# Kernel tuning notes

Measured on AMD Instinct MI355X. Metric: run time of the kernel, lower is better.

The kernel has to match this reference:

```python
import jax, jax.numpy as jnp
import numpy as np

N, D, F1, F2, F3, H = 4096, 512, 64, 32, 16, 4
ALPHA = 0.2  # LeakyReLU negative slope
NEG = -9e15


def setup_inputs() -> dict:
    key = jax.random.key(0)
    ks = jax.random.split(key, 11)
    # sparse binary adjacency with self loops (adj.to_dense() in original)
    adj = (jax.random.uniform(ks[1], (N, N)) < 0.01).astype(jnp.float32)
    adj = jnp.maximum(adj, jnp.eye(N, dtype=jnp.float32))
    return {
        "x": jax.random.normal(ks[0], (N, D), jnp.float32),
        "adj": adj,
        "W_heads": jax.random.normal(ks[2], (H, D, F1), jnp.float32) * 0.05,
        "a_heads": jax.random.normal(ks[3], (H, 2 * F1, 1), jnp.float32) * 0.05,
        "W_att": jax.random.normal(ks[4], (H * F1, F1), jnp.float32) * 0.05,
        "a_att": jax.random.normal(ks[5], (2 * F1, 1), jnp.float32) * 0.05,
        "W1": jax.random.normal(ks[6], (F1, F2), jnp.float32) * 0.05,
        "W2": jax.random.normal(ks[7], (F2, F3), jnp.float32) * 0.05,
        "W3": jax.random.normal(ks[8], (F2, F3), jnp.float32) * 0.05,
        "eps": jax.random.normal(ks[9], (N, F3), jnp.float32),
    }


def _gat(x, adj, W, a, out_dim):
    Wh = x @ W                                   # [N, F]
    e = (Wh @ a[:out_dim]) + (Wh @ a[out_dim:]).T  # [N,1] + [1,N] -> [N,N]
    e = jax.nn.leaky_relu(e, negative_slope=ALPHA)
    att = jax.nn.softmax(jnp.where(adj > 0, e, NEG), axis=-1)
    return jax.nn.elu(att @ Wh)                  # [N, F]


def reference(x, adj, W_heads, a_heads, W_att, a_att, W1, W2, W3, eps):
    # multi-head GAT, concat along feature dim
    heads = jax.vmap(lambda W, a: _gat(x, adj, W, a, F1))(W_heads, a_heads)  # [H,N,F1]
    cat = jnp.transpose(heads, (1, 0, 2)).reshape(N, H * F1)
    gc_att = _gat(cat, adj, W_att, a_att, F1)    # [N, F1]
    # GCN layers (dropout off, no bias): spmm(adj, x @ W)
    h1 = jax.nn.relu(adj @ (gc_att @ W1))        # [N, F2]
    mu = adj @ (h1 @ W2)                         # [N, F3]
    logvar = adj @ (h1 @ W3)                     # [N, F3]
    # reparameterize (vae_bool=True): eps * exp(logvar) + mu
    z = eps * jnp.exp(logvar) + mu
    adj_rec = z @ z.T                            # inner-product decoder [N,N]
    return adj_rec, mu, logvar
```

## Files before the change

### kernel.cpp

```cpp
#include <hip/hip_runtime.h>
#include <math.h>

#define NN 4096
#define DD 512
#define F1 64
#define F2 32
#define F3 16
#define NH 4
#define ALPHA 0.2f
#define CAP 160

__global__ void k_csr(const float* __restrict__ adj, int* __restrict__ colidx,
                      int* __restrict__ deg) {
  __shared__ int cnt;
  int i = blockIdx.x, tid = threadIdx.x;
  if (tid == 0) cnt = 0;
  __syncthreads();
  const float4* arow = (const float4*)(adj + (size_t)i * NN);
  for (int t = tid; t < NN / 4; t += 256) {
    float4 v = arow[t];
    int base = t * 4;
    if (v.x != 0.f) { int p = atomicAdd(&cnt, 1); if (p < CAP) colidx[(size_t)i * CAP + p] = base; }
    if (v.y != 0.f) { int p = atomicAdd(&cnt, 1); if (p < CAP) colidx[(size_t)i * CAP + p] = base + 1; }
    if (v.z != 0.f) { int p = atomicAdd(&cnt, 1); if (p < CAP) colidx[(size_t)i * CAP + p] = base + 2; }
    if (v.w != 0.f) { int p = atomicAdd(&cnt, 1); if (p < CAP) colidx[(size_t)i * CAP + p] = base + 3; }
  }
  __syncthreads();
  if (tid == 0) deg[i] = cnt < CAP ? cnt : CAP;
}

__global__ void k_wh_heads(const float* __restrict__ x,
                           const float* __restrict__ W_heads,
                           const float* __restrict__ a_heads,
                           float* __restrict__ Whcat,
                           float* __restrict__ s1,
                           float* __restrict__ s2) {
  const int ROWS = 4;
  __shared__ float xs[ROWS][DD];
  int tid = threadIdx.x;
  int r0 = blockIdx.x * ROWS;
  const float4* xsrc = (const float4*)(x + (size_t)r0 * DD);
  for (int t = tid; t < ROWS * DD / 4; t += 256) ((float4*)xs)[t] = xsrc[t];
  __syncthreads();
  int h = tid >> 6;
  int f = tid & 63;
  const float* W = W_heads + (size_t)h * DD * F1 + f;
  float acc[ROWS] = {0.f, 0.f, 0.f, 0.f};
  for (int k = 0; k < DD; k += 4) {
    float w0 = W[(k + 0) * F1];
    float w1 = W[(k + 1) * F1];
    float w2 = W[(k + 2) * F1];
    float w3 = W[(k + 3) * F1];
#pragma unroll
    for (int r = 0; r < ROWS; ++r) {
      float4 xv = *(const float4*)&xs[r][k];
      acc[r] = fmaf(xv.x, w0, acc[r]);
      acc[r] = fmaf(xv.y, w1, acc[r]);
      acc[r] = fmaf(xv.z, w2, acc[r]);
      acc[r] = fmaf(xv.w, w3, acc[r]);
    }
  }
  float a1 = a_heads[h * 2 * F1 + f];
  float a2 = a_heads[h * 2 * F1 + F1 + f];
#pragma unroll
  for (int r = 0; r < ROWS; ++r) {
    Whcat[(size_t)(r0 + r) * (NH * F1) + tid] = acc[r];
    float v1 = acc[r] * a1;
    float v2 = acc[r] * a2;
#pragma unroll
    for (int off = 32; off > 0; off >>= 1) {
      v1 += __shfl_down(v1, off, 64);
      v2 += __shfl_down(v2, off, 64);
    }
    if (f == 0) {
      s1[h * NN + r0 + r] = v1;
      s2[h * NN + r0 + r] = v2;
    }
  }
}

__global__ void k_gat_heads(const int* __restrict__ colidx, const int* __restrict__ deg,
                            const float* __restrict__ Whcat,
                            const float* __restrict__ s1, const float* __restrict__ s2,
                            float* __restrict__ cat) {
  __shared__ int idx[CAP];
  __shared__ float s2s[NH][CAP];
  int i = blockIdx.x, tid = threadIdx.x;
  int c = deg[i];
  for (int t = tid; t < c; t += 256) idx[t] = colidx[(size_t)i * CAP + t];
  __syncthreads();
  int h = tid >> 6;
  int f = tid & 63;
  const float* s2h = s2 + h * NN;
  for (int k = f; k < c; k += 64) s2s[h][k] = s2h[idx[k]];
  __syncthreads();
  float s1v = s1[h * NN + i];
  float M = -INFINITY;
  for (int k = f; k < c; k += 64) M = fmaxf(M, s2s[h][k]);
#pragma unroll
  for (int off = 32; off > 0; off >>= 1) M = fmaxf(M, __shfl_down(M, off, 64));
  M = __shfl(M, 0, 64);
  float e0 = s1v + M;
  float m = (e0 >= 0.f) ? e0 : ALPHA * e0;
  float acc = 0.f, l = 0.f;
  for (int k = 0; k < c; ++k) {
    int j = idx[k];
    float e = s1v + s2s[h][k];
    e = (e >= 0.f) ? e : ALPHA * e;
    float w = __expf(e - m);
    l += w;
    acc = fmaf(w, Whcat[(size_t)j * (NH * F1) + tid], acc);
  }
  float o = acc / l;
  cat[(size_t)i * (NH * F1) + tid] = (o > 0.f) ? o : expm1f(o);
}

__global__ void k_wh2(const float* __restrict__ cat,
                      const float* __restrict__ W_att,
                      const float* __restrict__ a_att,
                      float* __restrict__ Wh2,
                      float* __restrict__ s1b, float* __restrict__ s2b) {
  const int ROWS = 8;
  __shared__ float cs[ROWS][NH * F1];
  int tid = threadIdx.x;
  int r0 = blockIdx.x * ROWS;
  const float4* csrc = (const float4*)(cat + (size_t)r0 * 256);
  for (int t = tid; t < ROWS * 256 / 4; t += 256) ((float4*)cs)[t] = csrc[t];
  __syncthreads();
  int g = tid >> 6;
  int f = tid & 63;
  float a1 = a_att[f], a2 = a_att[64 + f];
  const float* W = W_att + f;
#pragma unroll
  for (int rr = 0; rr < 2; ++rr) {
    int r = g * 2 + rr;
    float acc = 0.f;
    for (int k = 0; k < 256; k += 4) {
      float4 cv = *(const float4*)&cs[r][k];
      acc = fmaf(cv.x, W[(k + 0) * 64], acc);
      acc = fmaf(cv.y, W[(k + 1) * 64], acc);
      acc = fmaf(cv.z, W[(k + 2) * 64], acc);
      acc = fmaf(cv.w, W[(k + 3) * 64], acc);
    }
    Wh2[(size_t)(r0 + r) * 64 + f] = acc;
    float v1 = acc * a1, v2 = acc * a2;
#pragma unroll
    for (int off = 32; off > 0; off >>= 1) {
      v1 += __shfl_down(v1, off, 64);
      v2 += __shfl_down(v2, off, 64);
    }
    if (f == 0) { s1b[r0 + r] = v1; s2b[r0 + r] = v2; }
  }
}

__global__ void k_gat2(const int* __restrict__ colidx, const int* __restrict__ deg,
                       const float* __restrict__ Wh2,
                       const float* __restrict__ s1b, const float* __restrict__ s2b,
                       float* __restrict__ gc) {
  __shared__ int idx[4][CAP];
  int w = threadIdx.x >> 6, f = threadIdx.x & 63;
  int i = blockIdx.x * 4 + w;
  int c = deg[i];
  for (int k = f; k < c; k += 64) idx[w][k] = colidx[(size_t)i * CAP + k];
  __syncthreads();
  float s1v = s1b[i];
  float M = -INFINITY;
  for (int k = f; k < c; k += 64) M = fmaxf(M, s2b[idx[w][k]]);
#pragma unroll
  for (int off = 32; off > 0; off >>= 1) M = fmaxf(M, __shfl_down(M, off, 64));
  M = __shfl(M, 0, 64);
  float e0 = s1v + M;
  float m = (e0 >= 0.f) ? e0 : ALPHA * e0;
  float acc = 0.f, l = 0.f;
  for (int k = 0; k < c; ++k) {
    int j = idx[w][k];
    float e = s1v + s2b[j];
    e = (e >= 0.f) ? e : ALPHA * e;
    float wt = __expf(e - m);
    l += wt;
    acc = fmaf(wt, Wh2[(size_t)j * 64 + f], acc);
  }
  float o = acc / l;
  gc[(size_t)i * 64 + f] = (o > 0.f) ? o : expm1f(o);
}

__global__ void k_t1(const float* __restrict__ gc, const float* __restrict__ W1,
                     float* __restrict__ t1) {
  const int ROWS = 8;
  __shared__ float gs[ROWS][64];
  int tid = threadIdx.x;
  int r0 = blockIdx.x * ROWS;
  const float4* gsrc = (const float4*)(gc + (size_t)r0 * 64);
  for (int t = tid; t < ROWS * 64 / 4; t += 256) ((float4*)gs)[t] = gsrc[t];
  __syncthreads();
  int r = tid >> 5, f = tid & 31;
  float acc = 0.f;
  for (int k = 0; k < 64; ++k) acc = fmaf(gs[r][k], W1[k * 32 + f], acc);
  t1[(size_t)(r0 + r) * 32 + f] = acc;
}

__global__ void k_gcn1(const int* __restrict__ colidx, const int* __restrict__ deg,
                       const float* __restrict__ t1, float* __restrict__ h1) {
  __shared__ int idx[8][CAP];
  int tid = threadIdx.x;
  int r = tid >> 5, lane = tid & 31;
  int i = blockIdx.x * 8 + r;
  int c = deg[i];
  for (int k = lane; k < c; k += 32) idx[r][k] = colidx[(size_t)i * CAP + k];
  __syncthreads();
  float acc = 0.f;
  for (int k = 0; k < c; ++k) acc += t1[(size_t)idx[r][k] * 32 + lane];
  h1[(size_t)i * 32 + lane] = fmaxf(acc, 0.f);
}

__global__ void k_t23(const float* __restrict__ h1, const float* __restrict__ W2,
                      const float* __restrict__ W3, float* __restrict__ t23) {
  const int ROWS = 8;
  __shared__ float hs[ROWS][32];
  int tid = threadIdx.x;
  int r0 = blockIdx.x * ROWS;
  const float4* hsrc = (const float4*)(h1 + (size_t)r0 * 32);
  for (int t = tid; t < ROWS * 32 / 4; t += 256) ((float4*)hs)[t] = hsrc[t];
  __syncthreads();
  int r = tid >> 5, f = tid & 31;
  const float* W = (f < 16) ? (W2 + f) : (W3 + (f - 16));
  float acc = 0.f;
  for (int k = 0; k < F2; ++k) acc = fmaf(hs[r][k], W[k * 16], acc);
  t23[(size_t)(r0 + r) * 32 + f] = acc;
}

__global__ void k_gcn2(const int* __restrict__ colidx, const int* __restrict__ deg,
                       const float* __restrict__ t23, const float* __restrict__ eps,
                       float* __restrict__ mu_out, float* __restrict__ lv_out,
                       float* __restrict__ z) {
  __shared__ int idx[8][CAP];
  int tid = threadIdx.x;
  int r = tid >> 5, g = tid & 31;
  int i = blockIdx.x * 8 + r;
  int c = deg[i];
  for (int k = g; k < c; k += 32) idx[r][k] = colidx[(size_t)i * CAP + k];
  __syncthreads();
  float acc = 0.f;
  for (int k = 0; k < c; ++k) acc += t23[(size_t)idx[r][k] * 32 + g];
  float lvv = __shfl(acc, (threadIdx.x & 63) + 16, 64);
  if (g < 16) {
    mu_out[(size_t)i * 16 + g] = acc;
    z[(size_t)i * 16 + g] = eps[(size_t)i * 16 + g] * expf(lvv) + acc;
  } else {
    lv_out[(size_t)i * 16 + (g - 16)] = acc;
  }
}

__global__ void k_zzt(const float* __restrict__ z, float* __restrict__ out) {
  __shared__ float zr[64][17];
  __shared__ float zc[64][17];
  int bj = blockIdx.x, bi = blockIdx.y;
  int tid = threadIdx.x;
  for (int t = tid; t < 64 * 16; t += 256) {
    zr[t >> 4][t & 15] = z[(size_t)(bi * 64 + (t >> 4)) * 16 + (t & 15)];
    zc[t >> 4][t & 15] = z[(size_t)(bj * 64 + (t >> 4)) * 16 + (t & 15)];
  }
  __syncthreads();
  int cthr = tid & 63;
  int rbase = (tid >> 6) * 16;
  for (int r = rbase; r < rbase + 16; ++r) {
    float acc = 0.f;
#pragma unroll
    for (int k = 0; k < 16; ++k) acc = fmaf(zr[r][k], zc[cthr][k], acc);
    out[(size_t)(bi * 64 + r) * NN + bj * 64 + cthr] = acc;
  }
}

extern "C" void kernel_launch(void* const* d_in, const int* in_sizes, int n_in,
                              void* d_out, int out_size, void* d_ws, size_t ws_size,
                              hipStream_t stream) {
  const float* x       = (const float*)d_in[0];
  const float* adj     = (const float*)d_in[1];
  const float* W_heads = (const float*)d_in[2];
  const float* a_heads = (const float*)d_in[3];
  const float* W_att   = (const float*)d_in[4];
  const float* a_att   = (const float*)d_in[5];
  const float* W1      = (const float*)d_in[6];
  const float* W2      = (const float*)d_in[7];
  const float* W3      = (const float*)d_in[8];
  const float* eps     = (const float*)d_in[9];

  float* out = (float*)d_out;
  float* adj_rec = out;
  float* mu_out  = out + (size_t)NN * NN;
  float* lv_out  = mu_out + (size_t)NN * F3;

  float* ws = (float*)d_ws;
  float* Whcat = ws;               ws += (size_t)NN * NH * F1;
  float* s1    = ws;               ws += (size_t)NH * NN;
  float* s2    = ws;               ws += (size_t)NH * NN;
  float* cat   = ws;               ws += (size_t)NN * NH * F1;
  float* Wh2   = ws;               ws += (size_t)NN * F1;
  float* s1b   = ws;               ws += NN;
  float* s2b   = ws;               ws += NN;
  float* gc    = ws;               ws += (size_t)NN * F1;
  float* t1    = ws;               ws += (size_t)NN * F2;
  float* h1    = ws;               ws += (size_t)NN * F2;
  float* t23   = ws;               ws += (size_t)NN * 2 * F3;
  float* z     = ws;               ws += (size_t)NN * F3;
  int*   colidx = (int*)ws;        ws += (size_t)NN * CAP;
  int*   deg    = (int*)ws;        ws += NN;

  k_csr<<<NN, 256, 0, stream>>>(adj, colidx, deg);
  k_wh_heads<<<NN / 4, 256, 0, stream>>>(x, W_heads, a_heads, Whcat, s1, s2);
  k_gat_heads<<<NN, 256, 0, stream>>>(colidx, deg, Whcat, s1, s2, cat);
  k_wh2<<<NN / 8, 256, 0, stream>>>(cat, W_att, a_att, Wh2, s1b, s2b);
  k_gat2<<<NN / 4, 256, 0, stream>>>(colidx, deg, Wh2, s1b, s2b, gc);
  k_t1<<<NN / 8, 256, 0, stream>>>(gc, W1, t1);
  k_gcn1<<<NN / 8, 256, 0, stream>>>(colidx, deg, t1, h1);
  k_t23<<<NN / 8, 256, 0, stream>>>(h1, W2, W3, t23);
  k_gcn2<<<NN / 8, 256, 0, stream>>>(colidx, deg, t23, eps, mu_out, lv_out, z);
  k_zzt<<<dim3(64, 64), 256, 0, stream>>>(z, adj_rec);
}
```

Baseline: 255.5 us.

## Fuse GAT/GCN stages, transpose head weights, and register-tile the decoder

Adds a kernel that transposes W_heads so the head projection can read contiguous float4 weights. The projection now runs 512-thread blocks with a split-K reduction through shared memory. The GAT kernels precompute softmax weights cooperatively and use four independent accumulators in the gather. The second GAT is fused with the W1 projection, and the first GCN with the W2/W3 projection, which removes two launches and two intermediate buffers. The z·zᵀ decoder uses 4x4 register tiles with float4 stores to cut the cost of writing the large output. An extra transpose launch is added in exchange.

```diff
diff --git a/kernel.cpp b/kernel.cpp
--- a/kernel.cpp
+++ b/kernel.cpp
@@ -10,6 +10,24 @@
 #define ALPHA 0.2f
 #define CAP 160
 
+__device__ __forceinline__ float lrelu(float e) { return (e >= 0.f) ? e : ALPHA * e; }
+
+__global__ void k_wtr(const float* __restrict__ W, float* __restrict__ Wt) {
+  __shared__ float tile[64][65];
+  int h = blockIdx.x >> 3;
+  int kt = (blockIdx.x & 7) * 64;
+  int tid = threadIdx.x;
+  for (int t = tid; t < 4096; t += 256) {
+    int kk = t >> 6, ff = t & 63;
+    tile[kk][ff] = W[(size_t)h * DD * F1 + (size_t)(kt + kk) * F1 + ff];
+  }
+  __syncthreads();
+  for (int t = tid; t < 4096; t += 256) {
+    int ff = t >> 6, kk = t & 63;
+    Wt[(size_t)(h * F1 + ff) * DD + kt + kk] = tile[kk][ff];
+  }
+}
+
 __global__ void k_csr(const float* __restrict__ adj, int* __restrict__ colidx,
                       int* __restrict__ deg) {
   __shared__ int cnt;
@@ -29,52 +47,88 @@
   if (tid == 0) deg[i] = cnt < CAP ? cnt : CAP;
 }
 
-__global__ void k_wh_heads(const float* __restrict__ x,
-                           const float* __restrict__ W_heads,
-                           const float* __restrict__ a_heads,
-                           float* __restrict__ Whcat,
-                           float* __restrict__ s1,
-                           float* __restrict__ s2) {
-  const int ROWS = 4;
-  __shared__ float xs[ROWS][DD];
-  int tid = threadIdx.x;
-  int r0 = blockIdx.x * ROWS;
+__global__ __launch_bounds__(512) void k_wh_heads(
+    const float* __restrict__ x, const float* __restrict__ Wt,
+    const float* __restrict__ a_heads, float* __restrict__ Whcat,
+    float* __restrict__ s1, float* __restrict__ s2) {
+  __shared__ float xs[8 * DD];
+  int tid = threadIdx.x;
+  int r0 = blockIdx.x * 8;
   const float4* xsrc = (const float4*)(x + (size_t)r0 * DD);
-  for (int t = tid; t < ROWS * DD / 4; t += 256) ((float4*)xs)[t] = xsrc[t];
-  __syncthreads();
-  int h = tid >> 6;
+  float4* xd = (float4*)xs;
+  xd[tid] = xsrc[tid];
+  xd[tid + 512] = xsrc[tid + 512];
+  __syncthreads();
   int f = tid & 63;
-  const float* W = W_heads + (size_t)h * DD * F1 + f;
-  float acc[ROWS] = {0.f, 0.f, 0.f, 0.f};
-  for (int k = 0; k < DD; k += 4) {
-    float w0 = W[(k + 0) * F1];
-    float w1 = W[(k + 1) * F1];
-    float w2 = W[(k + 2) * F1];
-    float w3 = W[(k + 3) * F1];
-#pragma unroll
-    for (int r = 0; r < ROWS; ++r) {
-      float4 xv = *(const float4*)&xs[r][k];
-      acc[r] = fmaf(xv.x, w0, acc[r]);
-      acc[r] = fmaf(xv.y, w1, acc[r]);
-      acc[r] = fmaf(xv.z, w2, acc[r]);
-      acc[r] = fmaf(xv.w, w3, acc[r]);
+  int rg = (tid >> 6) & 3;
+  int ks = tid >> 8;
+  int k0 = ks * 256;
+  const float* wp0 = Wt + (size_t)(0 * F1 + f) * DD;
+  const float* wp1 = Wt + (size_t)(1 * F1 + f) * DD;
+  const float* wp2 = Wt + (size_t)(2 * F1 + f) * DD;
+  const float* wp3 = Wt + (size_t)(3 * F1 + f) * DD;
+  const float* xa = xs + (size_t)(rg * 2) * DD;
+  const float* xb = xa + DD;
+  float acc[2][4] = {{0.f,0.f,0.f,0.f},{0.f,0.f,0.f,0.f}};
+  for (int k = k0; k < k0 + 256; k += 4) {
+    float4 wv[4];
+    wv[0] = *(const float4*)(wp0 + k);
+    wv[1] = *(const float4*)(wp1 + k);
+    wv[2] = *(const float4*)(wp2 + k);
+    wv[3] = *(const float4*)(wp3 + k);
+    float4 va = *(const float4*)(xa + k);
+    float4 vb = *(const float4*)(xb + k);
+#pragma unroll
+    for (int h = 0; h < 4; ++h) {
+      acc[0][h] = fmaf(va.x, wv[h].x, acc[0][h]);
+      acc[0][h] = fmaf(va.y, wv[h].y, acc[0][h]);
+      acc[0][h] = fmaf(va.z, wv[h].z, acc[0][h]);
+      acc[0][h] = fmaf(va.w, wv[h].w, acc[0][h]);
+      acc[1][h] = fmaf(vb.x, wv[h].x, acc[1][h]);
+      acc[1][h] = fmaf(vb.y, wv[h].y, acc[1][h]);
+      acc[1][h] = fmaf(vb.z, wv[h].z, acc[1][h]);
+      acc[1][h] = fmaf(vb.w, wv[h].w, acc[1][h]);
     }
   }
-  float a1 = a_heads[h * 2 * F1 + f];
-  float a2 = a_heads[h * 2 * F1 + F1 + f];
-#pragma unroll
-  for (int r = 0; r < ROWS; ++r) {
-    Whcat[(size_t)(r0 + r) * (NH * F1) + tid] = acc[r];
-    float v1 = acc[r] * a1;
-    float v2 = acc[r] * a2;
-#pragma unroll
-    for (int off = 32; off > 0; off >>= 1) {
-      v1 += __shfl_down(v1, off, 64);
-      v2 += __shfl_down(v2, off, 64);
-    }
-    if (f == 0) {
-      s1[h * NN + r0 + r] = v1;
-      s2[h * NN + r0 + r] = v2;
+  __syncthreads();
+  float* pbuf = xs;
+  if (ks == 1) {
+    int t = tid & 255;
+#pragma unroll
+    for (int r = 0; r < 2; ++r)
+#pragma unroll
+      for (int h = 0; h < 4; ++h) pbuf[t * 8 + r * 4 + h] = acc[r][h];
+  }
+  __syncthreads();
+  if (ks == 0) {
+#pragma unroll
+    for (int r = 0; r < 2; ++r)
+#pragma unroll
+      for (int h = 0; h < 4; ++h) acc[r][h] += pbuf[tid * 8 + r * 4 + h];
+    int rb = r0 + rg * 2;
+#pragma unroll
+    for (int r = 0; r < 2; ++r)
+#pragma unroll
+      for (int h = 0; h < 4; ++h)
+        Whcat[(size_t)(rb + r) * (NH * F1) + h * 64 + f] = acc[r][h];
+#pragma unroll
+    for (int h = 0; h < 4; ++h) {
+      float a1 = a_heads[h * 2 * F1 + f];
+      float a2 = a_heads[h * 2 * F1 + F1 + f];
+#pragma unroll
+      for (int r = 0; r < 2; ++r) {
+        float v1 = acc[r][h] * a1;
+        float v2 = acc[r][h] * a2;
+#pragma unroll
+        for (int off = 32; off > 0; off >>= 1) {
+          v1 += __shfl_down(v1, off, 64);
+          v2 += __shfl_down(v2, off, 64);
+        }
+        if (f == 0) {
+          s1[h * NN + rb + r] = v1;
+          s2[h * NN + rb + r] = v2;
+        }
+      }
     }
   }
 }
@@ -84,7 +138,7 @@
                             const float* __restrict__ s1, const float* __restrict__ s2,
                             float* __restrict__ cat) {
   __shared__ int idx[CAP];
-  __shared__ float s2s[NH][CAP];
+  __shared__ float wsh[NH][CAP];
   int i = blockIdx.x, tid = threadIdx.x;
   int c = deg[i];
   for (int t = tid; t < c; t += 256) idx[t] = colidx[(size_t)i * CAP + t];
@@ -92,26 +146,39 @@
   int h = tid >> 6;
   int f = tid & 63;
   const float* s2h = s2 + h * NN;
-  for (int k = f; k < c; k += 64) s2s[h][k] = s2h[idx[k]];
-  __syncthreads();
   float s1v = s1[h * NN + i];
   float M = -INFINITY;
-  for (int k = f; k < c; k += 64) M = fmaxf(M, s2s[h][k]);
+  for (int k = f; k < c; k += 64) {
+    float v = s2h[idx[k]];
+    wsh[h][k] = v;
+    M = fmaxf(M, v);
+  }
 #pragma unroll
   for (int off = 32; off > 0; off >>= 1) M = fmaxf(M, __shfl_down(M, off, 64));
   M = __shfl(M, 0, 64);
-  float e0 = s1v + M;
-  float m = (e0 >= 0.f) ? e0 : ALPHA * e0;
-  float acc = 0.f, l = 0.f;
-  for (int k = 0; k < c; ++k) {
-    int j = idx[k];
-    float e = s1v + s2s[h][k];
-    e = (e >= 0.f) ? e : ALPHA * e;
-    float w = __expf(e - m);
-    l += w;
-    acc = fmaf(w, Whcat[(size_t)j * (NH * F1) + tid], acc);
-  }
-  float o = acc / l;
+  float m = lrelu(s1v + M);
+  float lsum = 0.f;
+  for (int k = f; k < c; k += 64) {
+    float w = __expf(lrelu(s1v + wsh[h][k]) - m);
+    wsh[h][k] = w;
+    lsum += w;
+  }
+#pragma unroll
+  for (int off = 32; off > 0; off >>= 1) lsum += __shfl_down(lsum, off, 64);
+  float linv = 1.f / __shfl(lsum, 0, 64);
+  __syncthreads();
+  const float* base = Whcat + h * 64 + f;
+  float a0 = 0.f, a1 = 0.f, a2 = 0.f, a3 = 0.f;
+  int k = 0;
+  for (; k + 4 <= c; k += 4) {
+    int j0 = idx[k], j1 = idx[k + 1], j2 = idx[k + 2], j3 = idx[k + 3];
+    a0 = fmaf(wsh[h][k],     base[(size_t)j0 * 256], a0);
+    a1 = fmaf(wsh[h][k + 1], base[(size_t)j1 * 256], a1);
+    a2 = fmaf(wsh[h][k + 2], base[(size_t)j2 * 256], a2);
+    a3 = fmaf(wsh[h][k + 3], base[(size_t)j3 * 256], a3);
+  }
+  for (; k < c; ++k) a0 = fmaf(wsh[h][k], base[(size_t)idx[k] * 256], a0);
+  float o = (a0 + a1 + a2 + a3) * linv;
   cat[(size_t)i * (NH * F1) + tid] = (o > 0.f) ? o : expm1f(o);
 }
 
@@ -153,101 +220,129 @@
   }
 }
 
-__global__ void k_gat2(const int* __restrict__ colidx, const int* __restrict__ deg,
-                       const float* __restrict__ Wh2,
-                       const float* __restrict__ s1b, const float* __restrict__ s2b,
-                       float* __restrict__ gc) {
-  __shared__ int idx[4][CAP];
-  int w = threadIdx.x >> 6, f = threadIdx.x & 63;
+__global__ void k_gat2t1(const int* __restrict__ colidx, const int* __restrict__ deg,
+                         const float* __restrict__ Wh2,
+                         const float* __restrict__ s1b, const float* __restrict__ s2b,
+                         const float* __restrict__ W1, float* __restrict__ t1) {
+  __shared__ int idx4[4][CAP];
+  __shared__ float wsh4[4][CAP];
+  __shared__ float grow[4][64];
+  __shared__ float W1s[F1 * F2];
+  int tid = threadIdx.x;
+  int w = tid >> 6, f = tid & 63;
   int i = blockIdx.x * 4 + w;
   int c = deg[i];
-  for (int k = f; k < c; k += 64) idx[w][k] = colidx[(size_t)i * CAP + k];
+  for (int t = tid; t < F1 * F2; t += 256) W1s[t] = W1[t];
+  for (int k = f; k < c; k += 64) idx4[w][k] = colidx[(size_t)i * CAP + k];
   __syncthreads();
   float s1v = s1b[i];
   float M = -INFINITY;
-  for (int k = f; k < c; k += 64) M = fmaxf(M, s2b[idx[w][k]]);
+  for (int k = f; k < c; k += 64) {
+    float v = s2b[idx4[w][k]];
+    wsh4[w][k] = v;
+    M = fmaxf(M, v);
+  }
 #pragma unroll
   for (int off = 32; off > 0; off >>= 1) M = fmaxf(M, __shfl_down(M, off, 64));
   M = __shfl(M, 0, 64);
-  float e0 = s1v + M;
-  float m = (e0 >= 0.f) ? e0 : ALPHA * e0;
-  float acc = 0.f, l = 0.f;
-  for (int k = 0; k < c; ++k) {
-    int j = idx[w][k];
-    float e = s1v + s2b[j];
-    e = (e >= 0.f) ? e : ALPHA * e;
-    float wt = __expf(e - m);
-    l += wt;
-    acc = fmaf(wt, Wh2[(size_t)j * 64 + f], acc);
-  }
-  float o = acc / l;
-  gc[(size_t)i * 64 + f] = (o > 0.f) ? o : expm1f(o);
-}
-
-__global__ void k_t1(const float* __restrict__ gc, const float* __restrict__ W1,
-                     float* __restrict__ t1) {
-  const int ROWS = 8;
-  __shared__ float gs[ROWS][64];
-  int tid = threadIdx.x;
-  int r0 = blockIdx.x * ROWS;
-  const float4* gsrc = (const float4*)(gc + (size_t)r0 * 64);
-  for (int t = tid; t < ROWS * 64 / 4; t += 256) ((float4*)gs)[t] = gsrc[t];
-  __syncthreads();
-  int r = tid >> 5, f = tid & 31;
-  float acc = 0.f;
-  for (int k = 0; k < 64; ++k) acc = fmaf(gs[r][k], W1[k * 32 + f], acc);
-  t1[(size_t)(r0 + r) * 32 + f] = acc;
-}
-
-__global__ void k_gcn1(const int* __restrict__ colidx, const int* __restrict__ deg,
-                       const float* __restrict__ t1, float* __restrict__ h1) {
-  __shared__ int idx[8][CAP];
-  int tid = threadIdx.x;
-  int r = tid >> 5, lane = tid & 31;
-  int i = blockIdx.x * 8 + r;
+  float m = lrelu(s1v + M);
+  float lsum = 0.f;
+  for (int k = f; k < c; k += 64) {
+    float wv = __expf(lrelu(s1v + wsh4[w][k]) - m);
+    wsh4[w][k] = wv;
+    lsum += wv;
+  }
+#pragma unroll
+  for (int off = 32; off > 0; off >>= 1) lsum += __shfl_down(lsum, off, 64);
+  float linv = 1.f / __shfl(lsum, 0, 64);
+  __syncthreads();
+  const float* base = Wh2 + f;
+  float a0 = 0.f, a1 = 0.f, a2 = 0.f, a3 = 0.f;
+  int k = 0;
+  for (; k + 4 <= c; k += 4) {
+    int j0 = idx4[w][k], j1 = idx4[w][k + 1], j2 = idx4[w][k + 2], j3 = idx4[w][k + 3];
+    a0 = fmaf(wsh4[w][k],     base[(size_t)j0 * 64], a0);
+    a1 = fmaf(wsh4[w][k + 1], base[(size_t)j1 * 64], a1);
+    a2 = fmaf(wsh4[w][k + 2], base[(size_t)j2 * 64], a2);
+    a3 = fmaf(wsh4[w][k + 3], base[(size_t)j3 * 64], a3);
+  }
+  for (; k < c; ++k) a0 = fmaf(wsh4[w][k], base[(size_t)idx4[w][k] * 64], a0);
+  float o = (a0 + a1 + a2 + a3) * linv;
+  grow[w][f] = (o > 0.f) ? o : expm1f(o);
+  __syncthreads();
+  if (f < F2) {
+    float acc = 0.f;
+#pragma unroll 8
+    for (int kk = 0; kk < F1; ++kk) acc = fmaf(grow[w][kk], W1s[kk * F2 + f], acc);
+    t1[(size_t)i * F2 + f] = acc;
+  }
+}
+
+__global__ void k_gcn1t23(const int* __restrict__ colidx, const int* __restrict__ deg,
+                          const float* __restrict__ t1,
+                          const float* __restrict__ W2, const float* __restrict__ W3,
+                          float* __restrict__ t23) {
+  __shared__ int idx4[4][CAP];
+  __shared__ float hrow[4][F2];
+  __shared__ float Wc[F2 * 32];
+  int tid = threadIdx.x;
+  int w = tid >> 6, lane = tid & 63;
+  int nb = lane >> 5, g = lane & 31;
+  int i = blockIdx.x * 4 + w;
   int c = deg[i];
-  for (int k = lane; k < c; k += 32) idx[r][k] = colidx[(size_t)i * CAP + k];
-  __syncthreads();
-  float acc = 0.f;
-  for (int k = 0; k < c; ++k) acc += t1[(size_t)idx[r][k] * 32 + lane];
-  h1[(size_t)i * 32 + lane] = fmaxf(acc, 0.f);
-}
-
-__global__ void k_t23(const float* __restrict__ h1, const float* __restrict__ W2,
-                      const float* __restrict__ W3, float* __restrict__ t23) {
-  const int ROWS = 8;
-  __shared__ float hs[ROWS][32];
-  int tid = threadIdx.x;
-  int r0 = blockIdx.x * ROWS;
-  const float4* hsrc = (const float4*)(h1 + (size_t)r0 * 32);
-  for (int t = tid; t < ROWS * 32 / 4; t += 256) ((float4*)hs)[t] = hsrc[t];
-  __syncthreads();
-  int r = tid >> 5, f = tid & 31;
-  const float* W = (f < 16) ? (W2 + f) : (W3 + (f - 16));
-  float acc = 0.f;
-  for (int k = 0; k < F2; ++k) acc = fmaf(hs[r][k], W[k * 16], acc);
-  t23[(size_t)(r0 + r) * 32 + f] = acc;
+  for (int t = tid; t < F2 * 32; t += 256) {
+    int kk = t >> 5, gg = t & 31;
+    Wc[t] = (gg < 16) ? W2[kk * 16 + gg] : W3[kk * 16 + (gg - 16)];
+  }
+  for (int k = lane; k < c; k += 64) idx4[w][k] = colidx[(size_t)i * CAP + k];
+  __syncthreads();
+  float a0 = 0.f, a1 = 0.f;
+  int k = nb;
+  for (; k + 2 < c; k += 4) {
+    a0 += t1[(size_t)idx4[w][k] * F2 + g];
+    a1 += t1[(size_t)idx4[w][k + 2] * F2 + g];
+  }
+  for (; k < c; k += 2) a0 += t1[(size_t)idx4[w][k] * F2 + g];
+  float tot = a0 + a1;
+  tot += __shfl_xor(tot, 32, 64);
+  float h1v = fmaxf(tot, 0.f);
+  if (nb == 0) hrow[w][g] = h1v;
+  __syncthreads();
+  if (lane < 32) {
+    float acc = 0.f;
+#pragma unroll 8
+    for (int kk = 0; kk < F2; ++kk) acc = fmaf(hrow[w][kk], Wc[kk * 32 + lane], acc);
+    t23[(size_t)i * 32 + lane] = acc;
+  }
 }
 
 __global__ void k_gcn2(const int* __restrict__ colidx, const int* __restrict__ deg,
                        const float* __restrict__ t23, const float* __restrict__ eps,
                        float* __restrict__ mu_out, float* __restrict__ lv_out,
                        float* __restrict__ z) {
-  __shared__ int idx[8][CAP];
-  int tid = threadIdx.x;
-  int r = tid >> 5, g = tid & 31;
-  int i = blockIdx.x * 8 + r;
+  __shared__ int idx4[4][CAP];
+  int tid = threadIdx.x;
+  int w = tid >> 6, lane = tid & 63;
+  int nb = lane >> 5, g = lane & 31;
+  int i = blockIdx.x * 4 + w;
   int c = deg[i];
-  for (int k = g; k < c; k += 32) idx[r][k] = colidx[(size_t)i * CAP + k];
-  __syncthreads();
-  float acc = 0.f;
-  for (int k = 0; k < c; ++k) acc += t23[(size_t)idx[r][k] * 32 + g];
-  float lvv = __shfl(acc, (threadIdx.x & 63) + 16, 64);
-  if (g < 16) {
-    mu_out[(size_t)i * 16 + g] = acc;
-    z[(size_t)i * 16 + g] = eps[(size_t)i * 16 + g] * expf(lvv) + acc;
-  } else {
-    lv_out[(size_t)i * 16 + (g - 16)] = acc;
+  for (int k = lane; k < c; k += 64) idx4[w][k] = colidx[(size_t)i * CAP + k];
+  __syncthreads();
+  float a0 = 0.f, a1 = 0.f;
+  int k = nb;
+  for (; k + 2 < c; k += 4) {
+    a0 += t23[(size_t)idx4[w][k] * 32 + g];
+    a1 += t23[(size_t)idx4[w][k + 2] * 32 + g];
+  }
+  for (; k < c; k += 2) a0 += t23[(size_t)idx4[w][k] * 32 + g];
+  float tot = a0 + a1;
+  tot += __shfl_xor(tot, 32, 64);
+  float lvv = __shfl(tot, (lane & 31) + 16, 64);
+  if (lane < 16) {
+    mu_out[(size_t)i * 16 + g] = tot;
+    z[(size_t)i * 16 + g] = eps[(size_t)i * 16 + g] * expf(lvv) + tot;
+  } else if (lane < 32) {
+    lv_out[(size_t)i * 16 + (g - 16)] = tot;
   }
 }
 
@@ -257,17 +352,29 @@
   int bj = blockIdx.x, bi = blockIdx.y;
   int tid = threadIdx.x;
   for (int t = tid; t < 64 * 16; t += 256) {
-    zr[t >> 4][t & 15] = z[(size_t)(bi * 64 + (t >> 4)) * 16 + (t & 15)];
-    zc[t >> 4][t & 15] = z[(size_t)(bj * 64 + (t >> 4)) * 16 + (t & 15)];
-  }
-  __syncthreads();
-  int cthr = tid & 63;
-  int rbase = (tid >> 6) * 16;
-  for (int r = rbase; r < rbase + 16; ++r) {
-    float acc = 0.f;
-#pragma unroll
-    for (int k = 0; k < 16; ++k) acc = fmaf(zr[r][k], zc[cthr][k], acc);
-    out[(size_t)(bi * 64 + r) * NN + bj * 64 + cthr] = acc;
+    int r = t >> 4, kk = t & 15;
+    zr[r][kk] = z[(size_t)(bi * 64 + r) * 16 + kk];
+    zc[r][kk] = z[(size_t)(bj * 64 + r) * 16 + kk];
+  }
+  __syncthreads();
+  int rg = tid >> 4;
+  int cg = tid & 15;
+  float acc[4][4] = {};
+  for (int kk = 0; kk < 16; ++kk) {
+    float av[4], bv[4];
+#pragma unroll
+    for (int t = 0; t < 4; ++t) av[t] = zr[rg * 4 + t][kk];
+#pragma unroll
+    for (int t = 0; t < 4; ++t) bv[t] = zc[cg * 4 + t][kk];
+#pragma unroll
+    for (int r = 0; r < 4; ++r)
+#pragma unroll
+      for (int cc = 0; cc < 4; ++cc) acc[r][cc] = fmaf(av[r], bv[cc], acc[r][cc]);
+  }
+#pragma unroll
+  for (int r = 0; r < 4; ++r) {
+    float4 v = make_float4(acc[r][0], acc[r][1], acc[r][2], acc[r][3]);
+    *(float4*)&out[(size_t)(bi * 64 + rg * 4 + r) * NN + bj * 64 + cg * 4] = v;
   }
 }
 
@@ -298,22 +405,20 @@
   float* Wh2   = ws;               ws += (size_t)NN * F1;
   float* s1b   = ws;               ws += NN;
   float* s2b   = ws;               ws += NN;
-  float* gc    = ws;               ws += (size_t)NN * F1;
   float* t1    = ws;               ws += (size_t)NN * F2;
-  float* h1    = ws;               ws += (size_t)NN * F2;
   float* t23   = ws;               ws += (size_t)NN * 2 * F3;
   float* z     = ws;               ws += (size_t)NN * F3;
+  float* Wt    = ws;               ws += (size_t)NH * F1 * DD;
   int*   colidx = (int*)ws;        ws += (size_t)NN * CAP;
   int*   deg    = (int*)ws;        ws += NN;
 
+  k_wtr<<<32, 256, 0, stream>>>(W_heads, Wt);
   k_csr<<<NN, 256, 0, stream>>>(adj, colidx, deg);
-  k_wh_heads<<<NN / 4, 256, 0, stream>>>(x, W_heads, a_heads, Whcat, s1, s2);
+  k_wh_heads<<<NN / 8, 512, 0, stream>>>(x, Wt, a_heads, Whcat, s1, s2);
   k_gat_heads<<<NN, 256, 0, stream>>>(colidx, deg, Whcat, s1, s2, cat);
   k_wh2<<<NN / 8, 256, 0, stream>>>(cat, W_att, a_att, Wh2, s1b, s2b);
-  k_gat2<<<NN / 4, 256, 0, stream>>>(colidx, deg, Wh2, s1b, s2b, gc);
-  k_t1<<<NN / 8, 256, 0, stream>>>(gc, W1, t1);
-  k_gcn1<<<NN / 8, 256, 0, stream>>>(colidx, deg, t1, h1);
-  k_t23<<<NN / 8, 256, 0, stream>>>(h1, W2, W3, t23);
-  k_gcn2<<<NN / 8, 256, 0, stream>>>(colidx, deg, t23, eps, mu_out, lv_out, z);
+  k_gat2t1<<<NN / 4, 256, 0, stream>>>(colidx, deg, Wh2, s1b, s2b, W1, t1);
+  k_gcn1t23<<<NN / 4, 256, 0, stream>>>(colidx, deg, t1, W2, W3, t23);
+  k_gcn2<<<NN / 4, 256, 0, stream>>>(colidx, deg, t23, eps, mu_out, lv_out, z);
   k_zzt<<<dim3(64, 64), 256, 0, stream>>>(z, adj_rec);
 }
```

Result: slower. 332.1 us (+30.0%).
